# Performance work log

Measured on AMD Instinct MI355X. Metric: run time of the kernel, lower is better.

## Reference

```python
import jax, jax.numpy as jnp
import numpy as np

B, S, D = 8, 4096, 1024
H = 16
HD = D // H          # 64
FF = 128             # FeedForward default intermediate_size
EPS = 1e-6           # flax RMSNorm default


def _rmsnorm(x, g):
    return x * jax.lax.rsqrt(jnp.mean(x * x, axis=-1, keepdims=True) + EPS) * g


def setup_inputs() -> dict:
    key = jax.random.key(0)
    ks = jax.random.split(key, 12)
    s = 0.02
    return {
        "x": jax.random.normal(ks[0], (B, S, D), jnp.float32),
        "attention_mask": jnp.ones((B, HD), jnp.int32),
        # per-head QKV projections stacked over heads: [H, D, HD]
        "Wq": jax.random.normal(ks[1], (H, D, HD), jnp.float32) * s,
        "bq": jnp.zeros((H, HD), jnp.float32),
        "Wk": jax.random.normal(ks[2], (H, D, HD), jnp.float32) * s,
        "bk": jnp.zeros((H, HD), jnp.float32),
        "Wv": jax.random.normal(ks[3], (H, D, HD), jnp.float32) * s,
        "bv": jnp.zeros((H, HD), jnp.float32),
        "Wo": jax.random.normal(ks[4], (D, D), jnp.float32) * s,
        "bo": jnp.zeros((D,), jnp.float32),
        "W1": jax.random.normal(ks[5], (D, FF), jnp.float32) * s,
        "b1": jnp.zeros((FF,), jnp.float32),
        "W2": jax.random.normal(ks[6], (FF, D), jnp.float32) * s,
        "b2": jnp.zeros((D,), jnp.float32),
        "g1": jnp.ones((D,), jnp.float32),
        "g2": jnp.ones((D,), jnp.float32),
    }


def reference(x, attention_mask, Wq, bq, Wk, bk, Wv, bv, Wo, bo, W1, b1, W2, b2, g1, g2):
    # per-head projections, vectorized over heads: [B, H, S, HD]
    q = jnp.einsum('bsd,hde->bhse', x, Wq) + bq[:, None, :]
    k = jnp.einsum('bsd,hde->bhse', x, Wk) + bk[:, None, :]
    v = jnp.einsum('bsd,hde->bhse', x, Wv) + bv[:, None, :]
    # scores = k^T @ q -> [B, H, HD(kfeat), HD(qfeat)]  (feature-feature attention)
    scores = jnp.einsum('bhsk,bhsq->bhkq', k, q)
    # tiled mask: each row of [HD, HD] equals mask -> masks along last (q-feature) axis
    m = attention_mask[:, None, None, :]  # [B,1,1,HD]
    scores = jnp.where(m == 0, -jnp.inf, scores)
    w = jax.nn.softmax(scores / jnp.sqrt(jnp.float32(HD)), axis=-2)
    # out = v @ w -> [B, H, S, HD]
    attn = jnp.einsum('bhsk,bhkq->bhsq', v, w)
    attn = attn.transpose(0, 2, 1, 3).reshape(B, S, D)  # concat heads
    # output projection + residual + RMSNorm
    h = x + attn @ Wo + bo
    h = _rmsnorm(h, g1)
    # tanh FFN + residual + RMSNorm
    ff = jnp.tanh(h @ W1 + b1) @ W2 + b2
    out = _rmsnorm(h + ff, g2)
    return out
```

## Files before the change

kernel.cpp:

```cpp
#include <hip/hip_runtime.h>
#include <math.h>

typedef __attribute__((ext_vector_type(4))) float f32x4;
typedef __attribute__((ext_vector_type(8))) short short8;
typedef __attribute__((ext_vector_type(4))) short short4v;

__device__ __forceinline__ float b2f(unsigned short u) {
  unsigned int x = ((unsigned int)u) << 16;
  return __builtin_bit_cast(float, x);
}
__device__ __forceinline__ unsigned short f2b(float f) {
  unsigned int x = __builtin_bit_cast(unsigned int, f);
  x += 0x7fffu + ((x >> 16) & 1u);
  return (unsigned short)(x >> 16);
}

__device__ __forceinline__ void gload16(const unsigned short* g, unsigned short* l) {
  __builtin_amdgcn_global_load_lds(
      (__attribute__((address_space(1))) void*)(unsigned long long)(const void*)g,
      (__attribute__((address_space(3))) void*)l, 16, 0, 0);
}

#define BARR  { __builtin_amdgcn_sched_barrier(0); __builtin_amdgcn_s_barrier(); __builtin_amdgcn_sched_barrier(0); }
#define LBARR { __builtin_amdgcn_sched_barrier(0); asm volatile("s_waitcnt lgkmcnt(0)" ::: "memory"); __builtin_amdgcn_s_barrier(); __builtin_amdgcn_sched_barrier(0); }
#define VMW(n) { __builtin_amdgcn_sched_barrier(0); asm volatile("s_waitcnt vmcnt(" #n ")" ::: "memory"); __builtin_amdgcn_sched_barrier(0); }

__global__ __launch_bounds__(256) void prep_kernel(
    const float* __restrict__ x, unsigned short* __restrict__ xb,
    const float* __restrict__ Wq, const float* __restrict__ Wk,
    const float* __restrict__ Wv, const float* __restrict__ Wo,
    const float* __restrict__ W1, const float* __restrict__ W2,
    const float* __restrict__ bq, const float* __restrict__ bk, const float* __restrict__ bv,
    unsigned short* __restrict__ BqkvT, unsigned short* __restrict__ WoT,
    unsigned short* __restrict__ W1T, unsigned short* __restrict__ W2T,
    float* __restrict__ bqkv) {
  __shared__ float tile[64][65];
  int nb = blockIdx.x, t = threadIdx.x;
  if (nb < 16384) {
    long i = (long)nb * 256 + t;
    f32x4 a = ((const f32x4*)x)[i * 2];
    f32x4 b = ((const f32x4*)x)[i * 2 + 1];
    short8 o;
#pragma unroll
    for (int j = 0; j < 4; ++j) { o[j] = (short)f2b(a[j]); o[4 + j] = (short)f2b(b[j]); }
    ((short8*)xb)[i] = o;
    return;
  }
  int n0 = nb - 16384;
  if (n0 == 1088) {
#pragma unroll
    for (int it = 0; it < 12; ++it) {
      int idx = it * 256 + t;
      float v = (idx < 1024) ? bq[idx] : (idx < 2048 ? bk[idx - 1024] : bv[idx - 2048]);
      bqkv[idx] = v;
    }
    return;
  }
  const float* src; unsigned short* dst; int sld, dld;
  if (n0 < 768) {
    int w = n0 >> 8, rem = n0 & 255, h = rem >> 4, dc = rem & 15;
    const float* W = (w == 0) ? Wq : (w == 1 ? Wk : Wv);
    src = W + ((long)h * 1024 + dc * 64) * 64;                 sld = 64;
    dst = BqkvT + (long)(w * 1024 + h * 64) * 1024 + dc * 64;  dld = 1024;
  } else if (n0 < 1024) {
    int rem = n0 - 768, dr = rem >> 4, jc = rem & 15;
    src = Wo + (long)dr * 64 * 1024 + jc * 64;                 sld = 1024;
    dst = WoT + (long)jc * 64 * 1024 + dr * 64;                dld = 1024;
  } else if (n0 < 1056) {
    int rem = n0 - 1024, dr = rem >> 1, fc = rem & 1;
    src = W1 + (long)dr * 64 * 128 + fc * 64;                  sld = 128;
    dst = W1T + (long)fc * 64 * 1024 + dr * 64;                dld = 1024;
  } else {
    int rem = n0 - 1056, fr = rem >> 4, jc = rem & 15;
    src = W2 + (long)fr * 64 * 1024 + jc * 64;                 sld = 1024;
    dst = W2T + (long)jc * 64 * 128 + fr * 64;                 dld = 128;
  }
  int r = t >> 2, c0 = (t & 3) * 16;
#pragma unroll
  for (int j4 = 0; j4 < 4; ++j4) {
    f32x4 v = *(const f32x4*)(src + (long)r * sld + c0 + j4 * 4);
    tile[c0 + j4 * 4 + 0][r] = v[0];
    tile[c0 + j4 * 4 + 1][r] = v[1];
    tile[c0 + j4 * 4 + 2][r] = v[2];
    tile[c0 + j4 * 4 + 3][r] = v[3];
  }
  __syncthreads();
  short8 o0, o1;
#pragma unroll
  for (int j = 0; j < 8; ++j) {
    o0[j] = (short)f2b(tile[r][c0 + j]);
    o1[j] = (short)f2b(tile[r][c0 + 8 + j]);
  }
  *(short8*)(dst + (long)r * dld + c0) = o0;
  *(short8*)(dst + (long)r * dld + c0 + 8) = o1;
}

__device__ __forceinline__ void rdA2(short8 (&dst)[4][2], const char* paK0,
                                     const char* paK1, int off) {
#pragma unroll
  for (int fr = 0; fr < 4; ++fr) {
    dst[fr][0] = *(const short8*)(paK0 + off + fr * 2048);
    dst[fr][1] = *(const short8*)(paK1 + off + fr * 2048);
  }
}
__device__ __forceinline__ void rdB2(short8 (&dst)[2][2], const char* pbK0,
                                     const char* pbK1, int off) {
#pragma unroll
  for (int gr = 0; gr < 2; ++gr) {
    dst[gr][0] = *(const short8*)(pbK0 + off + gr * 2048);
    dst[gr][1] = *(const short8*)(pbK1 + off + gr * 2048);
  }
}
template <int BPH>
__device__ __forceinline__ void mfmaq_f(const short8 (&afr)[4][2], const short8 (&bf)[2][2],
                                        f32x4 (*ac)[4]) {
  __builtin_amdgcn_s_setprio(1);
#pragma unroll
  for (int fi = 0; fi < 4; ++fi)
#pragma unroll
    for (int gj = 0; gj < 2; ++gj)
#pragma unroll
      for (int ks = 0; ks < 2; ++ks)
        ac[fi][BPH * 2 + gj] = __builtin_amdgcn_mfma_f32_16x16x32_bf16(
            afr[fi][ks], bf[gj][ks], ac[fi][BPH * 2 + gj], 0, 0, 0);
  __builtin_amdgcn_s_setprio(0);
}

template <int EPI, int BSEL>
__global__ __launch_bounds__(512, 2) void gemm8p(
    const unsigned short* __restrict__ A, int lda,
    const unsigned short* __restrict__ Bt, int ldb,
    unsigned short* __restrict__ C, int ldc,
    const float* __restrict__ bias,
    const float* __restrict__ residf,
    const unsigned short* __restrict__ residb, int ldr,
    int K, int NBX) {
  extern __shared__ char smb[];
  const int tid = threadIdx.x;
  const int lane = tid & 63, wid = tid >> 6;
  const int wm = wid >> 2, wn = wid & 3;

  int nwg = gridDim.x, orig = blockIdx.x;
  int wg = ((orig & 7) * (nwg >> 3)) + (orig >> 3);
  const long m0 = (long)(wg / NBX) * 256;
  const long n0 = (long)(wg % NBX) * 256;
  const unsigned short* bt = BSEL ? (Bt + (m0 >> 12) * 1048576) : Bt;

  const int NT = K >> 6, NI = NT >> 1;

  const int lr = lane & 15, lc = (lane >> 4) * 16;
  const int eA = lc ^ ((lr & 7) << 4);
  const char* paK0 = smb + wm * 8192 + lr * 128 + eA;
  const char* paK1 = smb + wm * 8192 + lr * 128 + (eA ^ 64);
  const char* pbK0 = smb + 65536 + wn * 4096 + lr * 128 + eA;
  const char* pbK1 = smb + 65536 + wn * 4096 + lr * 128 + (eA ^ 64);

  short8 afr0[4][2], afr1[4][2];
  short8 bfr0[2][2], bfr1[2][2];
  f32x4 acc[8][4] = {};

  auto stA = [&](int buf, int ph, int kt) {
#pragma unroll
    for (int rnd = 0; rnd < 2; ++rnd) {
      int o = rnd * 8192 + tid * 16;
      int wms = o >> 13, rs = (o >> 7) & 63, cb = o & 127;
      int pcb = cb ^ ((rs & 7) << 4);
      const unsigned short* src = A + (m0 + wms * 128 + ph * 64 + rs) * (long)lda + kt * 64 + (pcb >> 1);
      gload16(src, (unsigned short*)(smb + buf * 32768 + ph * 16384 + o));
    }
  };
  auto stB = [&](int buf, int ph, int kt) {
#pragma unroll
    for (int rnd = 0; rnd < 2; ++rnd) {
      int o = rnd * 8192 + tid * 16;
      int wns = (o >> 12) & 3, rs = (o >> 7) & 31, cb = o & 127;
      int pcb = cb ^ ((rs & 7) << 4);
      const unsigned short* src = bt + (n0 + wns * 64 + ph * 32 + rs) * (long)ldb + kt * 64 + (pcb >> 1);
      gload16(src, (unsigned short*)(smb + 65536 + buf * 32768 + ph * 16384 + o));
    }
  };

  stA(0, 0, 0); stA(0, 1, 0); stB(0, 0, 0); stB(0, 1, 0);
  stA(1, 0, 1); stA(1, 1, 1); stB(1, 0, 1); stB(1, 1, 1);
  VMW(8);
  BARR;
  rdA2(afr0, paK0, paK1, 0);
  rdB2(bfr0, pbK0, pbK1, 0);

  for (int i = 0; i < NI; ++i) {
    int t2 = 2 * i + 2, t3 = 2 * i + 3;
    bool more = t2 < NT;
    LBARR;
    rdB2(bfr1, pbK0, pbK1, 16384);
    mfmaq_f<0>(afr0, bfr0, &acc[0]);
    LBARR;
    rdA2(afr1, paK0, paK1, 16384);
    mfmaq_f<1>(afr0, bfr1, &acc[0]);
    LBARR;
    if (more) { stA(0, 0, t2); stA(0, 1, t2); }
    mfmaq_f<0>(afr1, bfr0, &acc[4]);
    if (more) { VMW(4); } else { VMW(0); }
    LBARR;
    rdA2(afr0, paK0, paK1, 32768);
    rdB2(bfr0, pbK0, pbK1, 32768);
    if (more) { stB(0, 0, t2); stB(0, 1, t2); }
    mfmaq_f<1>(afr1, bfr1, &acc[4]);
    LBARR;
    rdB2(bfr1, pbK0, pbK1, 32768 + 16384);
    mfmaq_f<0>(afr0, bfr0, &acc[0]);
    LBARR;
    rdA2(afr1, paK0, paK1, 32768 + 16384);
    mfmaq_f<1>(afr0, bfr1, &acc[0]);
    LBARR;
    if (more) { stA(1, 0, t3); stA(1, 1, t3); }
    mfmaq_f<0>(afr1, bfr0, &acc[4]);
    if (more) { VMW(4); } else { VMW(0); }
    LBARR;
    if (more) { rdA2(afr0, paK0, paK1, 0); rdB2(bfr0, pbK0, pbK1, 0); }
    if (more) { stB(1, 0, t3); stB(1, 1, t3); }
    mfmaq_f<1>(afr1, bfr1, &acc[4]);
  }

#pragma unroll
  for (int f = 0; f < 8; ++f) {
#pragma unroll
    for (int g = 0; g < 4; ++g) {
      long col = n0 + wn * 64 + g * 16 + (lane & 15);
      float bv = bias[col];
#pragma unroll
      for (int r = 0; r < 4; ++r) {
        long row = m0 + wm * 128 + f * 16 + (lane >> 4) * 4 + r;
        float o = acc[f][g][r] + bv;
        if (EPI == 1) o += residf[row * (long)ldr + col];
        if (EPI == 3) o += b2f(residb[row * (long)ldr + col]);
        C[row * (long)ldc + col] = f2b(o);
      }
    }
  }
}

template <int EPI>
__global__ __launch_bounds__(256, 2) void gemm_bt(
    const unsigned short* __restrict__ A, int lda,
    const unsigned short* __restrict__ Bt, int ldb,
    unsigned short* __restrict__ C, int ldc,
    const float* __restrict__ bias, int K) {
  __shared__ __align__(16) unsigned short Asm[128 * 32];
  __shared__ __align__(16) unsigned short Bsm[128 * 32];
  const int tid = threadIdx.x;
  const int lane = tid & 63, wid = tid >> 6;
  const int wr = wid >> 1, wc = wid & 1;
  const long m0 = (long)blockIdx.y * 128;
  const long n0 = (long)blockIdx.x * 128;

  f32x4 acc[4][4] = {};

  for (int kk = 0; kk < K; kk += 32) {
    __syncthreads();
#pragma unroll
    for (int i = 0; i < 2; ++i) {
      int slot = i * 256 + tid;
      int r = slot >> 2, cg = (slot & 3) * 8;
      gload16(A + (m0 + r) * (long)lda + kk + cg, &Asm[slot * 8]);
      gload16(Bt + (n0 + r) * (long)ldb + kk + cg, &Bsm[slot * 8]);
    }
    __syncthreads();
    short8 af[4], bfr[4];
#pragma unroll
    for (int mt = 0; mt < 4; ++mt)
      af[mt] = *(const short8*)&Asm[(wr * 64 + mt * 16 + (lane & 15)) * 32 + (lane >> 4) * 8];
#pragma unroll
    for (int nt = 0; nt < 4; ++nt)
      bfr[nt] = *(const short8*)&Bsm[(wc * 64 + nt * 16 + (lane & 15)) * 32 + (lane >> 4) * 8];
#pragma unroll
    for (int mt = 0; mt < 4; ++mt)
#pragma unroll
      for (int nt = 0; nt < 4; ++nt)
        acc[mt][nt] = __builtin_amdgcn_mfma_f32_16x16x32_bf16(af[mt], bfr[nt], acc[mt][nt], 0, 0, 0);
  }

  const long row0 = m0 + wr * 64 + ((lane >> 4) * 4);
  const long col0 = n0 + wc * 64 + (lane & 15);
#pragma unroll
  for (int mt = 0; mt < 4; ++mt) {
#pragma unroll
    for (int nt = 0; nt < 4; ++nt) {
      long col = col0 + nt * 16;
      float bv = bias[col];
      f32x4 v = acc[mt][nt];
#pragma unroll
      for (int r = 0; r < 4; ++r) {
        long row = row0 + mt * 16 + r;
        float o = v[r] + bv;
        if (EPI == 2) o = tanhf(o);
        C[row * (long)ldc + col] = f2b(o);
      }
    }
  }
}

__device__ __forceinline__ int sperm(int e) { return ((e + (e >> 3)) & 7) << 4; }

__global__ __launch_bounds__(256) void scores_mfma(
    const unsigned short* __restrict__ QKV, float* __restrict__ part) {
  __shared__ __align__(16) char lds[32768];
  int bh = blockIdx.x, seg = blockIdx.y;
  int b = bh >> 4, h = bh & 15;
  int tid = threadIdx.x, lane = tid & 63, wid = tid >> 6;
  int e0 = (tid & 7) * 8;
  int sl0 = (tid >> 3) * 4;
  const unsigned short* Qg = QKV + h * 64;
  const unsigned short* Kg = QKV + 1024 + h * 64;
  f32x4 acc[4] = {};

  for (int ch = 0; ch < 8; ++ch) {
    long S0 = (long)b * 4096 + seg * 1024 + ch * 128;
    __syncthreads();
    short8 kv0 = *(const short8*)(Kg + (S0 + sl0 + 0) * 3072 + e0);
    short8 kv1 = *(const short8*)(Kg + (S0 + sl0 + 1) * 3072 + e0);
    short8 kv2 = *(const short8*)(Kg + (S0 + sl0 + 2) * 3072 + e0);
    short8 kv3 = *(const short8*)(Kg + (S0 + sl0 + 3) * 3072 + e0);
    short8 qv0 = *(const short8*)(Qg + (S0 + sl0 + 0) * 3072 + e0);
    short8 qv1 = *(const short8*)(Qg + (S0 + sl0 + 1) * 3072 + e0);
    short8 qv2 = *(const short8*)(Qg + (S0 + sl0 + 2) * 3072 + e0);
    short8 qv3 = *(const short8*)(Qg + (S0 + sl0 + 3) * 3072 + e0);
#pragma unroll
    for (int je = 0; je < 8; ++je) {
      int e = e0 + je;
      int sw = sperm(e);
      char* rowK = lds + e * 256;
      char* rowQ = lds + 16384 + e * 256;
      unsigned int klo = (unsigned short)kv0[je] | ((unsigned int)(unsigned short)kv1[je] << 16);
      unsigned int khi = (unsigned short)kv2[je] | ((unsigned int)(unsigned short)kv3[je] << 16);
      unsigned int qlo = (unsigned short)qv0[je] | ((unsigned int)(unsigned short)qv1[je] << 16);
      unsigned int qhi = (unsigned short)qv2[je] | ((unsigned int)(unsigned short)qv3[je] << 16);
      *(unsigned int*)(rowK + ((sl0 * 2) ^ sw)) = klo;
      *(unsigned int*)(rowK + ((sl0 * 2 + 4) ^ sw)) = khi;
      *(unsigned int*)(rowQ + ((sl0 * 2) ^ sw)) = qlo;
      *(unsigned int*)(rowQ + ((sl0 * 2 + 4) ^ sw)) = qhi;
    }
    __syncthreads();
#pragma unroll
    for (int ksi = 0; ksi < 4; ++ksi) {
      int colb = ksi * 64 + (lane >> 4) * 16;
      int erA = wid * 16 + (lane & 15);
      short8 af = *(const short8*)(lds + erA * 256 + (colb ^ sperm(erA)));
#pragma unroll
      for (int n = 0; n < 4; ++n) {
        int erB = n * 16 + (lane & 15);
        short8 bf = *(const short8*)(lds + 16384 + erB * 256 + (colb ^ sperm(erB)));
        acc[n] = __builtin_amdgcn_mfma_f32_16x16x32_bf16(af, bf, acc[n], 0, 0, 0);
      }
    }
  }
  float* dst = part + ((long)bh * 4 + seg) * 4096;
#pragma unroll
  for (int n = 0; n < 4; ++n)
#pragma unroll
    for (int r = 0; r < 4; ++r) {
      int k = wid * 16 + (lane >> 4) * 4 + r;
      int q = n * 16 + (lane & 15);
      dst[k * 64 + q] = acc[n][r];
    }
}

__global__ __launch_bounds__(64) void softmax_Wb(
    const float* __restrict__ part, const int* __restrict__ mask,
    unsigned short* __restrict__ Wb) {
  __shared__ float lt[64][65];
  int bh = blockIdx.x, q = threadIdx.x;
  int b = bh >> 4;
  const float* p0 = part + (long)bh * 4 * 4096;
  float s[64];
#pragma unroll
  for (int k = 0; k < 64; ++k)
    s[k] = p0[k * 64 + q] + p0[4096 + k * 64 + q] + p0[8192 + k * 64 + q] + p0[12288 + k * 64 + q];
  bool live = (mask[b * 64 + q] != 0);
  float m = -1e30f;
#pragma unroll
  for (int k = 0; k < 64; ++k) m = fmaxf(m, s[k]);
  float sum = 0.0f;
#pragma unroll
  for (int k = 0; k < 64; ++k) {
    s[k] = __expf((s[k] - m) * 0.125f);
    sum += s[k];
  }
  float inv = live ? 1.0f / sum : 0.0f;
#pragma unroll
  for (int k = 0; k < 64; ++k) lt[k][q] = s[k] * inv;
  __syncthreads();
  unsigned short* o = Wb + (long)bh * 4096 + q * 64;
#pragma unroll
  for (int j8 = 0; j8 < 8; ++j8) {
    short8 ov;
#pragma unroll
    for (int j = 0; j < 8; ++j) ov[j] = (short)f2b(lt[q][j8 * 8 + j]);
    *(short8*)(o + j8 * 8) = ov;
  }
}

__global__ __launch_bounds__(256) void wpt_kernel(
    const unsigned short* __restrict__ WoT, const unsigned short* __restrict__ Wb,
    unsigned short* __restrict__ WPT) {
  int dblk = blockIdx.x;
  int h = blockIdx.y;
  int b = blockIdx.z;
  int tid = threadIdx.x, lane = tid & 63, wid = tid >> 6;
  int d0 = dblk * 256 + wid * 64;
  const unsigned short* wb = Wb + (long)(b * 16 + h) * 4096;
  f32x4 acc[4][4] = {};
#pragma unroll
  for (int ks = 0; ks < 2; ++ks) {
    short8 bf[4];
#pragma unroll
    for (int nt = 0; nt < 4; ++nt)
      bf[nt] = *(const short8*)(wb + (nt * 16 + (lane & 15)) * 64 + ks * 32 + (lane >> 4) * 8);
#pragma unroll
    for (int mt = 0; mt < 4; ++mt) {
      short8 af = *(const short8*)(WoT + (long)(d0 + mt * 16 + (lane & 15)) * 1024 + h * 64 + ks * 32 + (lane >> 4) * 8);
#pragma unroll
      for (int nt = 0; nt < 4; ++nt)
        acc[mt][nt] = __builtin_amdgcn_mfma_f32_16x16x32_bf16(af, bf[nt], acc[mt][nt], 0, 0, 0);
    }
  }
#pragma unroll
  for (int mt = 0; mt < 4; ++mt)
#pragma unroll
    for (int nt = 0; nt < 4; ++nt)
#pragma unroll
      for (int r = 0; r < 4; ++r) {
        long row = d0 + mt * 16 + (lane >> 4) * 4 + r;
        int col = h * 64 + nt * 16 + (lane & 15);
        WPT[(long)b * 1048576 + row * 1024 + col] = f2b(acc[mt][nt][r]);
      }
}

template <int OUTF>
__global__ __launch_bounds__(256) void rmsnorm_k(
    const unsigned short* __restrict__ in, const float* __restrict__ g,
    unsigned short* __restrict__ outb, float* __restrict__ outf) {
  long row = blockIdx.x;
  int tid = threadIdx.x;
  short4v u = *(const short4v*)(in + row * 1024 + tid * 4);
  float v[4];
  float ss = 0.0f;
#pragma unroll
  for (int i = 0; i < 4; ++i) {
    v[i] = b2f((unsigned short)u[i]);
    ss += v[i] * v[i];
  }
#pragma unroll
  for (int off = 32; off > 0; off >>= 1) ss += __shfl_xor(ss, off, 64);
  __shared__ float wsum[4];
  if ((tid & 63) == 0) wsum[tid >> 6] = ss;
  __syncthreads();
  float tot = wsum[0] + wsum[1] + wsum[2] + wsum[3];
  float rs = rsqrtf(tot * (1.0f / 1024.0f) + 1e-6f);
  f32x4 gv = *(const f32x4*)(g + tid * 4);
  if (OUTF) {
    f32x4 ov;
#pragma unroll
    for (int i = 0; i < 4; ++i) ov[i] = v[i] * rs * gv[i];
    *(f32x4*)(outf + row * 1024 + tid * 4) = ov;
  } else {
    short4v ov;
#pragma unroll
    for (int i = 0; i < 4; ++i) ov[i] = (short)f2b(v[i] * rs * gv[i]);
    *(short4v*)(outb + row * 1024 + tid * 4) = ov;
  }
}

extern "C" void kernel_launch(void* const* d_in, const int* in_sizes, int n_in,
                              void* d_out, int out_size, void* d_ws, size_t ws_size,
                              hipStream_t stream) {
  const float* x  = (const float*)d_in[0];
  const int* mask = (const int*)d_in[1];
  const float* Wq = (const float*)d_in[2];
  const float* bq = (const float*)d_in[3];
  const float* Wk = (const float*)d_in[4];
  const float* bk = (const float*)d_in[5];
  const float* Wv = (const float*)d_in[6];
  const float* bv = (const float*)d_in[7];
  const float* Wo = (const float*)d_in[8];
  const float* bo = (const float*)d_in[9];
  const float* W1 = (const float*)d_in[10];
  const float* b1 = (const float*)d_in[11];
  const float* W2 = (const float*)d_in[12];
  const float* b2 = (const float*)d_in[13];
  const float* g1 = (const float*)d_in[14];
  const float* g2 = (const float*)d_in[15];

  char* ws = (char*)d_ws;
  size_t off = 0;
  auto alc = [&](size_t n) { size_t o = off; off += (n + 255) & ~(size_t)255; return o; };
  unsigned short* BqkvT = (unsigned short*)(ws + alc(3072UL * 1024 * 2));
  unsigned short* WoT   = (unsigned short*)(ws + alc(1024UL * 1024 * 2));
  unsigned short* W1T   = (unsigned short*)(ws + alc(128UL * 1024 * 2));
  unsigned short* W2T   = (unsigned short*)(ws + alc(1024UL * 128 * 2));
  float*          bqkv  = (float*)(ws + alc(3072UL * 4));
  unsigned short* R0    = (unsigned short*)(ws + alc(32768UL * 1024 * 2));
  unsigned short* R1    = (unsigned short*)(ws + alc(32768UL * 3072 * 2));
  unsigned short* R2    = (unsigned short*)(ws + alc(32768UL * 1024 * 2));
  unsigned short* Tb    = (unsigned short*)(ws + alc(32768UL * 128 * 2));
  float*          SP    = (float*)(ws + alc(512UL * 4096 * 4));
  unsigned short* Wbuf  = (unsigned short*)(ws + alc(128UL * 4096 * 2));
  if (ws_size < off) return;

  unsigned short* xb   = R0;
  unsigned short* WPT  = R0;
  unsigned short* HFb  = R0;
  unsigned short* QKVb = R1;
  unsigned short* H2b  = R1;
  unsigned short* H1b  = R2;
  float* outp = (float*)d_out;

  prep_kernel<<<17473, 256, 0, stream>>>(x, xb, Wq, Wk, Wv, Wo, W1, W2, bq, bk, bv,
                                         BqkvT, WoT, W1T, W2T, bqkv);
  gemm8p<0, 0><<<1536, 512, 131072, stream>>>(xb, 1024, BqkvT, 1024, QKVb, 3072,
                                              bqkv, nullptr, nullptr, 0, 1024, 12);
  scores_mfma<<<dim3(128, 4), 256, 0, stream>>>(QKVb, SP);
  softmax_Wb<<<128, 64, 0, stream>>>(SP, mask, Wbuf);
  wpt_kernel<<<dim3(4, 16, 8), 256, 0, stream>>>(WoT, Wbuf, WPT);
  gemm8p<1, 1><<<512, 512, 131072, stream>>>(QKVb + 2048, 3072, WPT, 1024, H1b, 1024,
                                             bo, x, nullptr, 1024, 1024, 4);
  rmsnorm_k<0><<<32768, 256, 0, stream>>>(H1b, g1, H2b, nullptr);
  gemm_bt<2><<<dim3(1, 256), 256, 0, stream>>>(H2b, 1024, W1T, 1024, Tb, 128, b1, 1024);
  gemm8p<3, 0><<<512, 512, 131072, stream>>>(Tb, 128, W2T, 128, HFb, 1024,
                                             b2, nullptr, H2b, 1024, 128, 4);
  rmsnorm_k<1><<<32768, 256, 0, stream>>>(HFb, g2, nullptr, outp);
}
```

Measured before the change: 533.8 us.

## Fold first RMSNorm into FFN GEMMs and reuse bf16 residual with new block mapping

The first RMSNorm no longer writes a normalized activation tensor. A small kernel computes only per-row inverse RMS scales. The g1 gain is folded into W1 during weight prep, and the row scale is applied inside the W1 GEMM epilogue before tanh and inside the W2 GEMM epilogue for the residual term. The attention output GEMM now reads its residual from the bf16 copy of x instead of fp32 x, which cuts memory traffic but adds rounding error. The large GEMM also gets a new workgroup-to-tile mapping that groups M tiles per XCD for cache locality.

```diff
diff --git a/kernel.cpp b/kernel.cpp
--- a/kernel.cpp
+++ b/kernel.cpp
@@ -31,6 +31,7 @@
     const float* __restrict__ Wv, const float* __restrict__ Wo,
     const float* __restrict__ W1, const float* __restrict__ W2,
     const float* __restrict__ bq, const float* __restrict__ bk, const float* __restrict__ bv,
+    const float* __restrict__ g1,
     unsigned short* __restrict__ BqkvT, unsigned short* __restrict__ WoT,
     unsigned short* __restrict__ W1T, unsigned short* __restrict__ W2T,
     float* __restrict__ bqkv) {
@@ -57,6 +58,7 @@
     return;
   }
   const float* src; unsigned short* dst; int sld, dld;
+  bool foldg = false; int dbase = 0;
   if (n0 < 768) {
     int w = n0 >> 8, rem = n0 & 255, h = rem >> 4, dc = rem & 15;
     const float* W = (w == 0) ? Wq : (w == 1 ? Wk : Wv);
@@ -70,6 +72,7 @@
     int rem = n0 - 1024, dr = rem >> 1, fc = rem & 1;
     src = W1 + (long)dr * 64 * 128 + fc * 64;                  sld = 128;
     dst = W1T + (long)fc * 64 * 1024 + dr * 64;                dld = 1024;
+    foldg = true; dbase = dr * 64;
   } else {
     int rem = n0 - 1056, fr = rem >> 4, jc = rem & 15;
     src = W2 + (long)fr * 64 * 1024 + jc * 64;                 sld = 1024;
@@ -88,8 +91,10 @@
   short8 o0, o1;
 #pragma unroll
   for (int j = 0; j < 8; ++j) {
-    o0[j] = (short)f2b(tile[r][c0 + j]);
-    o1[j] = (short)f2b(tile[r][c0 + 8 + j]);
+    float v0 = tile[r][c0 + j], v1 = tile[r][c0 + 8 + j];
+    if (foldg) { v0 *= g1[dbase + c0 + j]; v1 *= g1[dbase + c0 + 8 + j]; }
+    o0[j] = (short)f2b(v0);
+    o1[j] = (short)f2b(v1);
   }
   *(short8*)(dst + (long)r * dld + c0) = o0;
   *(short8*)(dst + (long)r * dld + c0 + 8) = o1;
@@ -134,16 +139,18 @@
     const float* __restrict__ bias,
     const float* __restrict__ residf,
     const unsigned short* __restrict__ residb, int ldr,
+    const float* __restrict__ rs, const float* __restrict__ g1f,
     int K, int NBX) {
   extern __shared__ char smb[];
   const int tid = threadIdx.x;
   const int lane = tid & 63, wid = tid >> 6;
   const int wm = wid >> 2, wn = wid & 3;
 
-  int nwg = gridDim.x, orig = blockIdx.x;
-  int wg = ((orig & 7) * (nwg >> 3)) + (orig >> 3);
-  const long m0 = (long)(wg / NBX) * 256;
-  const long n0 = (long)(wg % NBX) * 256;
+  int orig = blockIdx.x;
+  int xcd = orig & 7, j = orig >> 3;
+  int ms = j / (4 * NBX), nb = (j >> 2) % NBX, mq = j & 3;
+  const long m0 = (long)(xcd * 16 + ms * 4 + mq) * 256;
+  const long n0 = (long)nb * 256;
   const unsigned short* bt = BSEL ? (Bt + (m0 >> 12) * 1048576) : Bt;
 
   const int NT = K >> 6, NI = NT >> 1;
@@ -163,9 +170,9 @@
 #pragma unroll
     for (int rnd = 0; rnd < 2; ++rnd) {
       int o = rnd * 8192 + tid * 16;
-      int wms = o >> 13, rs = (o >> 7) & 63, cb = o & 127;
-      int pcb = cb ^ ((rs & 7) << 4);
-      const unsigned short* src = A + (m0 + wms * 128 + ph * 64 + rs) * (long)lda + kt * 64 + (pcb >> 1);
+      int wms = o >> 13, rsw = (o >> 7) & 63, cb = o & 127;
+      int pcb = cb ^ ((rsw & 7) << 4);
+      const unsigned short* src = A + (m0 + wms * 128 + ph * 64 + rsw) * (long)lda + kt * 64 + (pcb >> 1);
       gload16(src, (unsigned short*)(smb + buf * 32768 + ph * 16384 + o));
     }
   };
@@ -173,9 +180,9 @@
 #pragma unroll
     for (int rnd = 0; rnd < 2; ++rnd) {
       int o = rnd * 8192 + tid * 16;
-      int wns = (o >> 12) & 3, rs = (o >> 7) & 31, cb = o & 127;
-      int pcb = cb ^ ((rs & 7) << 4);
-      const unsigned short* src = bt + (n0 + wns * 64 + ph * 32 + rs) * (long)ldb + kt * 64 + (pcb >> 1);
+      int wns = (o >> 12) & 3, rsw = (o >> 7) & 31, cb = o & 127;
+      int pcb = cb ^ ((rsw & 7) << 4);
+      const unsigned short* src = bt + (n0 + wns * 64 + ph * 32 + rsw) * (long)ldb + kt * 64 + (pcb >> 1);
       gload16(src, (unsigned short*)(smb + 65536 + buf * 32768 + ph * 16384 + o));
     }
   };
@@ -227,12 +234,14 @@
     for (int g = 0; g < 4; ++g) {
       long col = n0 + wn * 64 + g * 16 + (lane & 15);
       float bv = bias[col];
+      float gv = (EPI == 5) ? g1f[col] : 0.0f;
 #pragma unroll
       for (int r = 0; r < 4; ++r) {
         long row = m0 + wm * 128 + f * 16 + (lane >> 4) * 4 + r;
         float o = acc[f][g][r] + bv;
         if (EPI == 1) o += residf[row * (long)ldr + col];
         if (EPI == 3) o += b2f(residb[row * (long)ldr + col]);
+        if (EPI == 5) o += b2f(residb[row * (long)ldr + col]) * rs[row] * gv;
         C[row * (long)ldc + col] = f2b(o);
       }
     }
@@ -244,7 +253,7 @@
     const unsigned short* __restrict__ A, int lda,
     const unsigned short* __restrict__ Bt, int ldb,
     unsigned short* __restrict__ C, int ldc,
-    const float* __restrict__ bias, int K) {
+    const float* __restrict__ bias, const float* __restrict__ rs, int K) {
   __shared__ __align__(16) unsigned short Asm[128 * 32];
   __shared__ __align__(16) unsigned short Bsm[128 * 32];
   const int tid = threadIdx.x;
@@ -291,8 +300,9 @@
 #pragma unroll
       for (int r = 0; r < 4; ++r) {
         long row = row0 + mt * 16 + r;
-        float o = v[r] + bv;
-        if (EPI == 2) o = tanhf(o);
+        float o = v[r];
+        if (EPI == 4) o = tanhf(o * rs[row] + bv);
+        else o += bv;
         C[row * (long)ldc + col] = f2b(o);
       }
     }
@@ -435,10 +445,31 @@
       }
 }
 
-template <int OUTF>
+__global__ __launch_bounds__(256) void rowscale_k(
+    const unsigned short* __restrict__ in, float* __restrict__ rs) {
+  long row = blockIdx.x;
+  int tid = threadIdx.x;
+  short4v u = *(const short4v*)(in + row * 1024 + tid * 4);
+  float ss = 0.0f;
+#pragma unroll
+  for (int i = 0; i < 4; ++i) {
+    float v = b2f((unsigned short)u[i]);
+    ss += v * v;
+  }
+#pragma unroll
+  for (int off = 32; off > 0; off >>= 1) ss += __shfl_xor(ss, off, 64);
+  __shared__ float wsum[4];
+  if ((tid & 63) == 0) wsum[tid >> 6] = ss;
+  __syncthreads();
+  if (tid == 0) {
+    float tot = wsum[0] + wsum[1] + wsum[2] + wsum[3];
+    rs[row] = rsqrtf(tot * (1.0f / 1024.0f) + 1e-6f);
+  }
+}
+
 __global__ __launch_bounds__(256) void rmsnorm_k(
     const unsigned short* __restrict__ in, const float* __restrict__ g,
-    unsigned short* __restrict__ outb, float* __restrict__ outf) {
+    float* __restrict__ outf) {
   long row = blockIdx.x;
   int tid = threadIdx.x;
   short4v u = *(const short4v*)(in + row * 1024 + tid * 4);
@@ -455,19 +486,12 @@
   if ((tid & 63) == 0) wsum[tid >> 6] = ss;
   __syncthreads();
   float tot = wsum[0] + wsum[1] + wsum[2] + wsum[3];
-  float rs = rsqrtf(tot * (1.0f / 1024.0f) + 1e-6f);
+  float rsv = rsqrtf(tot * (1.0f / 1024.0f) + 1e-6f);
   f32x4 gv = *(const f32x4*)(g + tid * 4);
-  if (OUTF) {
-    f32x4 ov;
-#pragma unroll
-    for (int i = 0; i < 4; ++i) ov[i] = v[i] * rs * gv[i];
-    *(f32x4*)(outf + row * 1024 + tid * 4) = ov;
-  } else {
-    short4v ov;
-#pragma unroll
-    for (int i = 0; i < 4; ++i) ov[i] = (short)f2b(v[i] * rs * gv[i]);
-    *(short4v*)(outb + row * 1024 + tid * 4) = ov;
-  }
+  f32x4 ov;
+#pragma unroll
+  for (int i = 0; i < 4; ++i) ov[i] = v[i] * rsv * gv[i];
+  *(f32x4*)(outf + row * 1024 + tid * 4) = ov;
 }
 
 extern "C" void kernel_launch(void* const* d_in, const int* in_sizes, int n_in,
@@ -501,31 +525,34 @@
   unsigned short* R0    = (unsigned short*)(ws + alc(32768UL * 1024 * 2));
   unsigned short* R1    = (unsigned short*)(ws + alc(32768UL * 3072 * 2));
   unsigned short* R2    = (unsigned short*)(ws + alc(32768UL * 1024 * 2));
+  unsigned short* WPb   = (unsigned short*)(ws + alc(8UL * 1024 * 1024 * 2));
   unsigned short* Tb    = (unsigned short*)(ws + alc(32768UL * 128 * 2));
   float*          SP    = (float*)(ws + alc(512UL * 4096 * 4));
   unsigned short* Wbuf  = (unsigned short*)(ws + alc(128UL * 4096 * 2));
+  float*          RSb   = (float*)(ws + alc(32768UL * 4));
   if (ws_size < off) return;
 
   unsigned short* xb   = R0;
-  unsigned short* WPT  = R0;
   unsigned short* HFb  = R0;
   unsigned short* QKVb = R1;
-  unsigned short* H2b  = R1;
   unsigned short* H1b  = R2;
   float* outp = (float*)d_out;
 
-  prep_kernel<<<17473, 256, 0, stream>>>(x, xb, Wq, Wk, Wv, Wo, W1, W2, bq, bk, bv,
+  prep_kernel<<<17473, 256, 0, stream>>>(x, xb, Wq, Wk, Wv, Wo, W1, W2, bq, bk, bv, g1,
                                          BqkvT, WoT, W1T, W2T, bqkv);
   gemm8p<0, 0><<<1536, 512, 131072, stream>>>(xb, 1024, BqkvT, 1024, QKVb, 3072,
-                                              bqkv, nullptr, nullptr, 0, 1024, 12);
+                                              bqkv, nullptr, nullptr, 0, nullptr, nullptr,
+                                              1024, 12);
   scores_mfma<<<dim3(128, 4), 256, 0, stream>>>(QKVb, SP);
   softmax_Wb<<<128, 64, 0, stream>>>(SP, mask, Wbuf);
-  wpt_kernel<<<dim3(4, 16, 8), 256, 0, stream>>>(WoT, Wbuf, WPT);
-  gemm8p<1, 1><<<512, 512, 131072, stream>>>(QKVb + 2048, 3072, WPT, 1024, H1b, 1024,
-                                             bo, x, nullptr, 1024, 1024, 4);
-  rmsnorm_k<0><<<32768, 256, 0, stream>>>(H1b, g1, H2b, nullptr);
-  gemm_bt<2><<<dim3(1, 256), 256, 0, stream>>>(H2b, 1024, W1T, 1024, Tb, 128, b1, 1024);
-  gemm8p<3, 0><<<512, 512, 131072, stream>>>(Tb, 128, W2T, 128, HFb, 1024,
-                                             b2, nullptr, H2b, 1024, 128, 4);
-  rmsnorm_k<1><<<32768, 256, 0, stream>>>(HFb, g2, nullptr, outp);
-}
+  wpt_kernel<<<dim3(4, 16, 8), 256, 0, stream>>>(WoT, Wbuf, WPb);
+  gemm8p<3, 1><<<512, 512, 131072, stream>>>(QKVb + 2048, 3072, WPb, 1024, H1b, 1024,
+                                             bo, nullptr, xb, 1024, nullptr, nullptr,
+                                             1024, 4);
+  rowscale_k<<<32768, 256, 0, stream>>>(H1b, RSb);
+  gemm_bt<4><<<dim3(1, 256), 256, 0, stream>>>(H1b, 1024, W1T, 1024, Tb, 128, b1, RSb, 1024);
+  gemm8p<5, 0><<<512, 512, 131072, stream>>>(Tb, 128, W2T, 128, HFb, 1024,
+                                             b2, nullptr, H1b, 1024, RSb, g1,
+                                             128, 4);
+  rmsnorm_k<<<32768, 256, 0, stream>>>(HFb, g2, outp);
+}
```

Result: faster. 508.7 us (-4.7%).
